# Kernel tuning notes

Measured on AMD Instinct MI355X. Metric: run time of the kernel, lower is better.

## Reference

```python
import jax, jax.numpy as jnp
import numpy as np

LN_EPS = 1e-5

def layer_norm(x, w, b):
    mu = jnp.mean(x, axis=-1, keepdims=True)
    var = jnp.var(x, axis=-1, keepdims=True)
    return (x - mu) * jax.lax.rsqrt(var + LN_EPS) * w + b

def masked_softmax_topk(ctx, k):
    # ctx: [B, D, D]; keep top-k per row (scatter-style mask), softmax over last dim
    B, D, _ = ctx.shape
    idx = jax.lax.top_k(ctx, k)[1]                       # [B, D, k]
    mask = jnp.zeros(ctx.shape, bool).at[
        jnp.arange(B)[:, None, None], jnp.arange(D)[None, :, None], idx
    ].set(True)
    return jax.nn.softmax(jnp.where(mask, ctx, -jnp.inf), axis=-1)

def setup_inputs() -> dict:
    key = jax.random.key(0)
    ks = jax.random.split(key, 8)
    B, H, W, C = 8, 96, 96, 256
    x1 = jax.random.normal(ks[0], (B, H, W, C), jnp.float32)
    x2 = jax.random.normal(ks[1], (B, H, W, C), jnp.float32)
    norm1_w = jnp.ones((C,), jnp.float32)
    norm1_b = jnp.zeros((C,), jnp.float32)
    reproj_w = jax.random.normal(ks[2], (2 * C, C), jnp.float32) * (1.0 / np.sqrt(C))  # 1x1 conv
    reproj_b = jnp.zeros((2 * C,), jnp.float32)
    norm2_w = jnp.ones((2 * C,), jnp.float32)
    norm2_b = jnp.zeros((2 * C,), jnp.float32)
    attn_w = jnp.full((4,), 0.25, jnp.float32)  # attn1..attn4 scalars
    return {"x1": x1, "x2": x2, "norm1_w": norm1_w, "norm1_b": norm1_b,
            "reproj_w": reproj_w, "reproj_b": reproj_b,
            "norm2_w": norm2_w, "norm2_b": norm2_b, "attn_w": attn_w}

def reference(x1, x2, norm1_w, norm1_b, reproj_w, reproj_b, norm2_w, norm2_b, attn_w):
    B, H, W, C = x1.shape
    N, D = H * W, C  # head_count = 1
    n1 = layer_norm(x1.reshape(B, N, C), norm1_w, norm1_b)   # values source
    n2 = layer_norm(x2.reshape(B, N, C), norm1_w, norm1_b)   # keys/queries source
    kq = jnp.swapaxes(n2, 1, 2)                              # [B, D, N]
    values = jnp.swapaxes(n1, 1, 2)                          # [B, D, N]
    keyv = jax.nn.softmax(kq, axis=2)                        # softmax over N
    query = jax.nn.softmax(kq, axis=1)                       # softmax over channels
    context = jnp.einsum('bdn,ben->bde', keyv, values)       # [B, D, D]
    ks = [D // 2, (D * 2) // 3, (D * 3) // 4, (D * 4) // 5]
    attended = jnp.zeros((B, D, N), x1.dtype)
    for i, k in enumerate(ks):
        attn = masked_softmax_topk(context, k)               # [B, D, D]
        attended = attended + attn_w[i] * jnp.einsum('bde,ben->bdn', attn, query)
    # 1x1 conv reprojection D -> 2D, then LayerNorm over 2D
    rp = jnp.einsum('od,bdn->bno', reproj_w, attended) + reproj_b  # [B, N, 2D]
    rp = layer_norm(rp, norm2_w, norm2_b)
    out = rp.reshape(B, H, W, 2 * C).transpose(0, 3, 1, 2)   # [B, 2C, H, W]
    return out
```

## Files before the change

### kernel.cpp

```cpp
#include <hip/hip_runtime.h>
#include <math.h>

typedef __attribute__((ext_vector_type(8))) short short8;
typedef __attribute__((ext_vector_type(4))) float f32x4;
typedef unsigned short u16;
typedef unsigned int u32;

constexpr int Bb = 8;
constexpr int Nn = 9216;
constexpr int Cc = 256;
constexpr int Oo = 512;
constexpr float LN_EPS = 1e-5f;
constexpr int KS2 = 8;

static __device__ __forceinline__ u16 f2bf(float f) {
    unsigned u = __builtin_bit_cast(unsigned, f);
    u += 0x7fffu + ((u >> 16) & 1u);
    return (u16)(u >> 16);
}
static __device__ __forceinline__ float bf2f(u16 u) {
    return __builtin_bit_cast(float, (unsigned)u << 16);
}

__global__ __launch_bounds__(512, 2) void k_pre(const float* __restrict__ src,
                                                const float* __restrict__ lnw,
                                                const float* __restrict__ lnb,
                                                u16* __restrict__ dstT,
                                                u16* __restrict__ Qexp,
                                                float* __restrict__ pS,
                                                int doExp) {
    __shared__ u16 tile[256][66];
    __shared__ float wsh[256], bsh[256];
    const int b = blockIdx.z;
    const int nc = (blockIdx.x & 7) * 18 + (blockIdx.x >> 3);
    const int n0 = nc * 64;
    const int t = threadIdx.x;
    if (t < 256) { wsh[t] = lnw[t]; bsh[t] = lnb[t]; }
    __syncthreads();

    const int r = t >> 3;
    const int g = t & 7;
    const long long row = (long long)b * Nn + n0 + r;
    const float* rowp = src + row * Cc;

    float4 v[8];
#pragma unroll
    for (int i = 0; i < 8; ++i)
        v[i] = *reinterpret_cast<const float4*>(rowp + g * 4 + i * 32);

    float s = 0.f, q = 0.f;
#pragma unroll
    for (int i = 0; i < 8; ++i) {
        s += v[i].x + v[i].y + v[i].z + v[i].w;
        q += v[i].x * v[i].x + v[i].y * v[i].y + v[i].z * v[i].z + v[i].w * v[i].w;
    }
    s += __shfl_xor(s, 1); s += __shfl_xor(s, 2); s += __shfl_xor(s, 4);
    q += __shfl_xor(q, 1); q += __shfl_xor(q, 2); q += __shfl_xor(q, 4);
    const float mu = s * (1.0f / Cc);
    const float rstd = rsqrtf(q * (1.0f / Cc) - mu * mu + LN_EPS);

    float se = 0.f;
#pragma unroll
    for (int i = 0; i < 8; ++i) {
        const int d = g * 4 + i * 32;
        const float4 w4 = *reinterpret_cast<const float4*>(&wsh[d]);
        const float4 b4 = *reinterpret_cast<const float4*>(&bsh[d]);
        v[i].x = (v[i].x - mu) * rstd * w4.x + b4.x;
        v[i].y = (v[i].y - mu) * rstd * w4.y + b4.y;
        v[i].z = (v[i].z - mu) * rstd * w4.z + b4.z;
        v[i].w = (v[i].w - mu) * rstd * w4.w + b4.w;
        if (doExp) {
            v[i].x = __expf(v[i].x); v[i].y = __expf(v[i].y);
            v[i].z = __expf(v[i].z); v[i].w = __expf(v[i].w);
            se += v[i].x + v[i].y + v[i].z + v[i].w;
        }
        tile[d + 0][r] = f2bf(v[i].x);
        tile[d + 1][r] = f2bf(v[i].y);
        tile[d + 2][r] = f2bf(v[i].z);
        tile[d + 3][r] = f2bf(v[i].w);
    }

    if (doExp) {
        se += __shfl_xor(se, 1); se += __shfl_xor(se, 2); se += __shfl_xor(se, 4);
        const float inv = 1.0f / se;
#pragma unroll
        for (int i = 0; i < 8; ++i) {
            const int d = g * 4 + i * 32;
            int2 pk;
            pk.x = (int)((unsigned)f2bf(v[i].x * inv) | ((unsigned)f2bf(v[i].y * inv) << 16));
            pk.y = (int)((unsigned)f2bf(v[i].z * inv) | ((unsigned)f2bf(v[i].w * inv) << 16));
            *reinterpret_cast<int2*>(Qexp + row * Cc + d) = pk;
        }
    }
    __syncthreads();

#pragma unroll
    for (int p = 0; p < 4; ++p) {
        const int d = p * 64 + (t >> 3);
        const int c = (t & 7) * 8;
        int4 u;
        u.x = (int)*reinterpret_cast<const u32*>(&tile[d][c + 0]);
        u.y = (int)*reinterpret_cast<const u32*>(&tile[d][c + 2]);
        u.z = (int)*reinterpret_cast<const u32*>(&tile[d][c + 4]);
        u.w = (int)*reinterpret_cast<const u32*>(&tile[d][c + 6]);
        *reinterpret_cast<int4*>(dstT + ((long long)(b * Cc + d)) * Nn + n0 + c) = u;
        if (doExp) {
            const unsigned uu[4] = {(unsigned)u.x, (unsigned)u.y, (unsigned)u.z, (unsigned)u.w};
            float ss = 0.f;
#pragma unroll
            for (int j = 0; j < 4; ++j) {
                ss += bf2f((u16)(uu[j] & 0xffff));
                ss += bf2f((u16)(uu[j] >> 16));
            }
            ss += __shfl_xor(ss, 1);
            ss += __shfl_xor(ss, 2);
            ss += __shfl_xor(ss, 4);
            if ((t & 7) == 0) pS[((long long)b * 144 + nc) * Cc + d] = ss;
        }
    }
}

__global__ __launch_bounds__(256) void k_colcomb(const float* __restrict__ pS,
                                                 float* __restrict__ colS) {
    const int d = threadIdx.x, b = blockIdx.x;
    float s = 0.f;
    for (int c = 0; c < 144; ++c) s += pS[((long long)b * 144 + c) * Cc + d];
    colS[b * Cc + d] = s;
}

__global__ __launch_bounds__(256) void k_mm_bf16(const u16* __restrict__ A,
                                                 const u16* __restrict__ Bt,
                                                 float* __restrict__ C,
                                                 int lda, int ldb, int ldc,
                                                 long long sAb, long long sBb, long long sCb,
                                                 int kChunk, long long sCk,
                                                 int tilesN, int kIters) {
    __shared__ alignas(16) unsigned char smemRaw[32768];
    u16* Asm = reinterpret_cast<u16*>(smemRaw);
    u16* Bsm = reinterpret_cast<u16*>(smemRaw + 16384);
    float (*patch)[16][68] = reinterpret_cast<float (*)[16][68]>(smemRaw);

    const int t = threadIdx.x;
    const int b = blockIdx.z, kc = blockIdx.y;
    const int tm = blockIdx.x / tilesN, tn = blockIdx.x % tilesN;
    const int m0 = tm * 128, n0 = tn * 128;
    const u16* Ag = A + b * sAb + (long long)kc * kChunk;
    const u16* Bg = Bt + b * sBb + (long long)kc * kChunk;
    float* Cg = C + b * sCb + (long long)kc * sCk;

    const int l = t & 63, w = t >> 6;
    const int wr = w >> 1, wc = w & 1;
    const int frow = l & 15, fk = (l >> 4) << 3;

    f32x4 acc[4][4] = {};

    for (int kt = 0; kt < kIters; ++kt) {
        const int k0 = kt * 64;
        int4 av[4], bv[4];
#pragma unroll
        for (int i = 0; i < 4; ++i) {
            const int s = t + 256 * i;
            const int r = s >> 3, c16 = s & 7;
            av[i] = *reinterpret_cast<const int4*>(Ag + (long long)(m0 + r) * lda + k0 + c16 * 8);
            bv[i] = *reinterpret_cast<const int4*>(Bg + (long long)(n0 + r) * ldb + k0 + c16 * 8);
        }
        __syncthreads();
#pragma unroll
        for (int i = 0; i < 4; ++i) {
            const int s = t + 256 * i;
            const int r = s >> 3, c16 = s & 7;
            const int idx = r * 64 + ((c16 * 8) ^ ((r & 7) << 3));
            *reinterpret_cast<int4*>(&Asm[idx]) = av[i];
            *reinterpret_cast<int4*>(&Bsm[idx]) = bv[i];
        }
        __syncthreads();
#pragma unroll
        for (int kf = 0; kf < 2; ++kf) {
            short8 af[4], bf[4];
            const int kk = kf * 32 + fk;
#pragma unroll
            for (int mi = 0; mi < 4; ++mi) {
                const int row = wr * 64 + mi * 16 + frow;
                af[mi] = *reinterpret_cast<const short8*>(&Asm[row * 64 + (kk ^ ((row & 7) << 3))]);
            }
#pragma unroll
            for (int ni = 0; ni < 4; ++ni) {
                const int row = wc * 64 + ni * 16 + frow;
                bf[ni] = *reinterpret_cast<const short8*>(&Bsm[row * 64 + (kk ^ ((row & 7) << 3))]);
            }
#pragma unroll
            for (int mi = 0; mi < 4; ++mi)
#pragma unroll
                for (int ni = 0; ni < 4; ++ni)
                    acc[mi][ni] = __builtin_amdgcn_mfma_f32_16x16x32_bf16(af[mi], bf[ni], acc[mi][ni], 0, 0, 0);
        }
    }

    __syncthreads();
    const int crow0 = (l >> 4) * 4, ccol = l & 15;
#pragma unroll
    for (int mi = 0; mi < 4; ++mi) {
#pragma unroll
        for (int ni = 0; ni < 4; ++ni)
#pragma unroll
            for (int r_ = 0; r_ < 4; ++r_)
                patch[w][crow0 + r_][ni * 16 + ccol] = acc[mi][ni][r_];
        asm volatile("s_waitcnt lgkmcnt(0)" ::: "memory");
        __builtin_amdgcn_sched_barrier(0);
#pragma unroll
        for (int row = 0; row < 16; ++row)
            Cg[(long long)(m0 + wr * 64 + mi * 16 + row) * ldc + n0 + wc * 64 + l] = patch[w][row][l];
        asm volatile("s_waitcnt lgkmcnt(0)" ::: "memory");
        __builtin_amdgcn_sched_barrier(0);
    }
}

__global__ __launch_bounds__(256) void k_ctxred(const float* __restrict__ ctxp,
                                                const float* __restrict__ colS,
                                                float* __restrict__ ctx) {
    const long long i4 = ((long long)blockIdx.x * 256 + threadIdx.x) * 4;
    float4 s = make_float4(0.f, 0.f, 0.f, 0.f);
    for (int kc = 0; kc < KS2; ++kc) {
        const float4 v = *reinterpret_cast<const float4*>(ctxp + (long long)kc * (Bb * Cc * Cc) + i4);
        s.x += v.x; s.y += v.y; s.z += v.z; s.w += v.w;
    }
    const int b = (int)(i4 >> 16);
    const int d = ((int)(i4 >> 8)) & 255;
    const float inv = 1.0f / colS[b * Cc + d];
    s.x *= inv; s.y *= inv; s.z *= inv; s.w *= inv;
    *reinterpret_cast<float4*>(ctx + i4) = s;
}

__global__ __launch_bounds__(256) void k_rank(const float* __restrict__ ctx,
                                              const float* __restrict__ aw,
                                              float* __restrict__ Ac) {
    __shared__ float row[256];
    __shared__ float red[256];
    const int d = blockIdx.x, b = blockIdx.y, e = threadIdx.x;
    const float c = ctx[((long long)(b * Cc + d)) * Cc + e];
    row[e] = c;
    __syncthreads();
    int p = 0;
    for (int j = 0; j < 256; ++j) {
        const float cj = row[j];
        p += (cj > c) || (cj == c && j < e);
    }
    red[e] = c; __syncthreads();
    for (int s_ = 128; s_; s_ >>= 1) { if (e < s_) red[e] = fmaxf(red[e], red[e + s_]); __syncthreads(); }
    const float m = red[0];
    const float ex = __expf(c - m);
    const int kks[4] = {128, 170, 192, 204};
    float Zv[4];
#pragma unroll
    for (int i = 0; i < 4; ++i) {
        __syncthreads();
        red[e] = (p < kks[i]) ? ex : 0.0f;
        __syncthreads();
        for (int s_ = 128; s_; s_ >>= 1) { if (e < s_) red[e] += red[e + s_]; __syncthreads(); }
        Zv[i] = red[0];
    }
    float wsum = 0.0f;
#pragma unroll
    for (int i = 0; i < 4; ++i)
        if (p < kks[i]) wsum += aw[i] / Zv[i];
    Ac[((long long)(b * Cc + d)) * Cc + e] = ex * wsum;
}

__global__ __launch_bounds__(256) void k_wa(const float* __restrict__ W,
                                            const float* __restrict__ Ac,
                                            u16* __restrict__ WAb16) {
    __shared__ float As[16][64], Bs[16][64];
    const int b = blockIdx.y;
    const int o0 = (blockIdx.x >> 2) * 64, e0 = (blockIdx.x & 3) * 64;
    const int t = threadIdx.x, tx = t & 15, ty = t >> 4;
    const int a_oo = t >> 2, a_k4 = (t & 3) * 4;
    const int b_kk = t >> 4, b_e4 = (t & 15) * 4;
    float acc[4][4] = {{0.f}};
    for (int kd = 0; kd < 256; kd += 16) {
        const float4 wv = *reinterpret_cast<const float4*>(W + (o0 + a_oo) * Cc + kd + a_k4);
        const float4 av = *reinterpret_cast<const float4*>(Ac + ((long long)(b * Cc + kd + b_kk)) * Cc + e0 + b_e4);
        __syncthreads();
        As[a_k4 + 0][a_oo] = wv.x; As[a_k4 + 1][a_oo] = wv.y;
        As[a_k4 + 2][a_oo] = wv.z; As[a_k4 + 3][a_oo] = wv.w;
        *reinterpret_cast<float4*>(&Bs[b_kk][b_e4]) = av;
        __syncthreads();
#pragma unroll
        for (int kk = 0; kk < 16; ++kk) {
            const float4 a4 = *reinterpret_cast<const float4*>(&As[kk][ty * 4]);
            const float4 b4 = *reinterpret_cast<const float4*>(&Bs[kk][tx * 4]);
            const float aa[4] = {a4.x, a4.y, a4.z, a4.w};
            const float bb[4] = {b4.x, b4.y, b4.z, b4.w};
#pragma unroll
            for (int i = 0; i < 4; ++i)
#pragma unroll
                for (int j = 0; j < 4; ++j) acc[i][j] = fmaf(aa[i], bb[j], acc[i][j]);
        }
    }
#pragma unroll
    for (int i = 0; i < 4; ++i) {
        int2 pk;
        pk.x = (int)((unsigned)f2bf(acc[i][0]) | ((unsigned)f2bf(acc[i][1]) << 16));
        pk.y = (int)((unsigned)f2bf(acc[i][2]) | ((unsigned)f2bf(acc[i][3]) << 16));
        *reinterpret_cast<int2*>(WAb16 + ((long long)(b * Oo + o0 + ty * 4 + i)) * Cc + e0 + tx * 4) = pk;
    }
}

__global__ __launch_bounds__(256, 3) void k_rpln(const u16* __restrict__ Qexp,
                                                 const u16* __restrict__ WAb16,
                                                 const float* __restrict__ rbias,
                                                 const float* __restrict__ nw,
                                                 const float* __restrict__ nb,
                                                 float* __restrict__ out) {
    __shared__ float patch[4][16][36];
    __shared__ float psum[32][4], psq[32][4];
    __shared__ float muA[32], rsA[32];

    const int t = threadIdx.x;
    const int b = blockIdx.z;
    const int nt_ = (blockIdx.x & 7) * 36 + (blockIdx.x >> 3);
    const int n0 = nt_ * 32;
    const int l = t & 63, w = t >> 6;
    const int frow = l & 15, fk = (l >> 4) << 3;
    const int hi = l >> 4;

    f32x4 acc[2][8] = {};

    const u16* Aq = Qexp + ((long long)b * Nn + n0) * Cc;
    const u16* Bw = WAb16 + ((long long)b * Oo + w * 128) * Cc;

    int4 aF[2][8];
#pragma unroll
    for (int mi = 0; mi < 2; ++mi)
#pragma unroll
        for (int s = 0; s < 8; ++s)
            aF[mi][s] = *reinterpret_cast<const int4*>(Aq + (mi * 16 + frow) * Cc + s * 32 + fk);

    int4 bC[8], bN[8];
#pragma unroll
    for (int ni = 0; ni < 8; ++ni)
        bC[ni] = *reinterpret_cast<const int4*>(Bw + (ni * 16 + frow) * Cc + fk);

#pragma unroll
    for (int s = 0; s < 8; ++s) {
        if (s < 7) {
            const int kk = (s + 1) * 32 + fk;
#pragma unroll
            for (int ni = 0; ni < 8; ++ni)
                bN[ni] = *reinterpret_cast<const int4*>(Bw + (ni * 16 + frow) * Cc + kk);
        }
#pragma unroll
        for (int mi = 0; mi < 2; ++mi)
#pragma unroll
            for (int ni = 0; ni < 8; ++ni)
                acc[mi][ni] = __builtin_amdgcn_mfma_f32_16x16x32_bf16(
                    __builtin_bit_cast(short8, aF[mi][s]), __builtin_bit_cast(short8, bC[ni]),
                    acc[mi][ni], 0, 0, 0);
        if (s < 7) {
#pragma unroll
            for (int ni = 0; ni < 8; ++ni) bC[ni] = bN[ni];
        }
    }

#pragma unroll
    for (int ni = 0; ni < 8; ++ni) {
        const float bb = rbias[w * 128 + ni * 16 + frow];
#pragma unroll
        for (int mi = 0; mi < 2; ++mi)
#pragma unroll
            for (int r_ = 0; r_ < 4; ++r_) acc[mi][ni][r_] += bb;
    }
#pragma unroll
    for (int mi = 0; mi < 2; ++mi)
#pragma unroll
        for (int r_ = 0; r_ < 4; ++r_) {
            float s = 0.f, q = 0.f;
#pragma unroll
            for (int ni = 0; ni < 8; ++ni) { const float v = acc[mi][ni][r_]; s += v; q += v * v; }
#pragma unroll
            for (int m = 8; m; m >>= 1) { s += __shfl_xor(s, m); q += __shfl_xor(q, m); }
            if (frow == 0) {
                const int row = mi * 16 + hi * 4 + r_;
                psum[row][w] = s; psq[row][w] = q;
            }
        }
    __syncthreads();
    if (t < 32) {
        const float s = psum[t][0] + psum[t][1] + psum[t][2] + psum[t][3];
        const float q = psq[t][0] + psq[t][1] + psq[t][2] + psq[t][3];
        const float m = s * (1.0f / Oo);
        muA[t] = m;
        rsA[t] = rsqrtf(q * (1.0f / Oo) - m * m + LN_EPS);
    }
    __syncthreads();

    float nwv[8], nbv[8];
#pragma unroll
    for (int ni = 0; ni < 8; ++ni) {
        const int o = w * 128 + ni * 16 + frow;
        nwv[ni] = nw[o]; nbv[ni] = nb[o];
    }

#pragma unroll
    for (int ni = 0; ni < 8; ++ni) {
#pragma unroll
        for (int mi = 0; mi < 2; ++mi)
#pragma unroll
            for (int r_ = 0; r_ < 4; ++r_) {
                const int nl = mi * 16 + hi * 4 + r_;
                patch[w][frow][nl] = (acc[mi][ni][r_] - muA[nl]) * rsA[nl] * nwv[ni] + nbv[ni];
            }
        asm volatile("s_waitcnt lgkmcnt(0)" ::: "memory");
        __builtin_amdgcn_sched_barrier(0);
#pragma unroll
        for (int p = 0; p < 2; ++p) {
            const int o_loc = p * 8 + (l >> 3);
            const int colf4 = l & 7;
            const f32x4 v = *reinterpret_cast<const f32x4*>(&patch[w][o_loc][colf4 * 4]);
            const int o_g = w * 128 + ni * 16 + o_loc;
            __builtin_nontemporal_store(v,
                reinterpret_cast<f32x4*>(&out[((long long)(b * Oo + o_g)) * Nn + n0 + colf4 * 4]));
        }
        asm volatile("s_waitcnt lgkmcnt(0)" ::: "memory");
        __builtin_amdgcn_sched_barrier(0);
    }
}

extern "C" void kernel_launch(void* const* d_in, const int* in_sizes, int n_in,
                              void* d_out, int out_size, void* d_ws, size_t ws_size,
                              hipStream_t stream) {
    (void)in_sizes; (void)n_in; (void)out_size; (void)ws_size;
    const float* x1    = (const float*)d_in[0];
    const float* x2    = (const float*)d_in[1];
    const float* n1w   = (const float*)d_in[2];
    const float* n1b   = (const float*)d_in[3];
    const float* rw    = (const float*)d_in[4];
    const float* rbias = (const float*)d_in[5];
    const float* n2w   = (const float*)d_in[6];
    const float* n2b   = (const float*)d_in[7];
    const float* aw    = (const float*)d_in[8];
    float* out = (float*)d_out;

    u16* KexpT = (u16*)d_out;
    u16* VT    = KexpT + (size_t)Bb * Nn * Cc;

    float* ws = (float*)d_ws;
    size_t off = 0;
    u16*   Qexp   = (u16*)(ws + off); off += (size_t)Bb * Nn * Cc / 2;
    float* ctxp   = ws + off; off += (size_t)KS2 * Bb * Cc * Cc;
    float* ctx    = ws + off; off += (size_t)Bb * Cc * Cc;
    float* Ac     = ws + off; off += (size_t)Bb * Cc * Cc;
    u16*   WAb16  = (u16*)(ws + off); off += (size_t)Bb * Oo * Cc / 2;
    float* pS     = ws + off; off += (size_t)Bb * 144 * Cc;
    float* colS   = ws + off; off += (size_t)Bb * Cc;

    k_pre<<<dim3(144, 1, Bb), 512, 0, stream>>>(x2, n1w, n1b, KexpT, Qexp, pS, 1);
    k_pre<<<dim3(144, 1, Bb), 512, 0, stream>>>(x1, n1w, n1b, VT, Qexp, pS, 0);
    k_colcomb<<<dim3(Bb), 256, 0, stream>>>(pS, colS);
    k_mm_bf16<<<dim3(4, KS2, Bb), 256, 0, stream>>>(
        KexpT, VT, ctxp,
        Nn, Nn, Cc,
        (long long)Cc * Nn, (long long)Cc * Nn, (long long)Cc * Cc,
        Nn / KS2, (long long)Bb * Cc * Cc,
        Cc / 128, (Nn / KS2) / 64);
    k_ctxred<<<dim3(512), 256, 0, stream>>>(ctxp, colS, ctx);
    k_rank<<<dim3(Cc, Bb), 256, 0, stream>>>(ctx, aw, Ac);
    k_wa<<<dim3(32, Bb), 256, 0, stream>>>(rw, Ac, WAb16);
    k_rpln<<<dim3(288, 1, Bb), 256, 0, stream>>>(Qexp, WAb16, rbias, n2w, n2b, out);
}
```

Baseline: 258.7 us.

## Store K/V row-major, drop Qexp buffer, fold row normalisation into reprojection

The preprocessing kernel now writes exp'd keys and values in row-major [N,C] bf16 instead of transposing through shared memory, and it no longer writes a separate row-normalised Qexp buffer. It stores per-row exp sums instead, and the reprojection kernel multiplies its output by the inverse row sum before adding the bias. The context GEMM transposes tiles while staging into shared memory, using scalar 16-bit LDS stores. This removes one full bf16 activation write and the LDS transpose in the prepass, at the cost of a more expensive shared-memory store pattern in the GEMM.

```diff
diff --git a/kernel.cpp b/kernel.cpp
--- a/kernel.cpp
+++ b/kernel.cpp
@@ -25,12 +25,12 @@
 __global__ __launch_bounds__(512, 2) void k_pre(const float* __restrict__ src,
                                                 const float* __restrict__ lnw,
                                                 const float* __restrict__ lnb,
-                                                u16* __restrict__ dstT,
-                                                u16* __restrict__ Qexp,
+                                                u16* __restrict__ dst,
+                                                float* __restrict__ rowsum,
                                                 float* __restrict__ pS,
                                                 int doExp) {
-    __shared__ u16 tile[256][66];
     __shared__ float wsh[256], bsh[256];
+    __shared__ float wred[8][256];
     const int b = blockIdx.z;
     const int nc = (blockIdx.x & 7) * 18 + (blockIdx.x >> 3);
     const int n0 = nc * 64;
@@ -40,6 +40,7 @@
 
     const int r = t >> 3;
     const int g = t & 7;
+    const int wv = t >> 6;
     const long long row = (long long)b * Nn + n0 + r;
     const float* rowp = src + row * Cc;
 
@@ -60,6 +61,7 @@
     const float rstd = rsqrtf(q * (1.0f / Cc) - mu * mu + LN_EPS);
 
     float se = 0.f;
+    u16 h[8][4];
 #pragma unroll
     for (int i = 0; i < 8; ++i) {
         const int d = g * 4 + i * 32;
@@ -74,48 +76,38 @@
             v[i].z = __expf(v[i].z); v[i].w = __expf(v[i].w);
             se += v[i].x + v[i].y + v[i].z + v[i].w;
         }
-        tile[d + 0][r] = f2bf(v[i].x);
-        tile[d + 1][r] = f2bf(v[i].y);
-        tile[d + 2][r] = f2bf(v[i].z);
-        tile[d + 3][r] = f2bf(v[i].w);
+        h[i][0] = f2bf(v[i].x); h[i][1] = f2bf(v[i].y);
+        h[i][2] = f2bf(v[i].z); h[i][3] = f2bf(v[i].w);
+        int2 pk;
+        pk.x = (int)((unsigned)h[i][0] | ((unsigned)h[i][1] << 16));
+        pk.y = (int)((unsigned)h[i][2] | ((unsigned)h[i][3] << 16));
+        *reinterpret_cast<int2*>(dst + row * Cc + d) = pk;
     }
 
     if (doExp) {
         se += __shfl_xor(se, 1); se += __shfl_xor(se, 2); se += __shfl_xor(se, 4);
-        const float inv = 1.0f / se;
+        if (g == 0) rowsum[row] = se;
 #pragma unroll
         for (int i = 0; i < 8; ++i) {
-            const int d = g * 4 + i * 32;
-            int2 pk;
-            pk.x = (int)((unsigned)f2bf(v[i].x * inv) | ((unsigned)f2bf(v[i].y * inv) << 16));
-            pk.y = (int)((unsigned)f2bf(v[i].z * inv) | ((unsigned)f2bf(v[i].w * inv) << 16));
-            *reinterpret_cast<int2*>(Qexp + row * Cc + d) = pk;
-        }
-    }
-    __syncthreads();
-
-#pragma unroll
-    for (int p = 0; p < 4; ++p) {
-        const int d = p * 64 + (t >> 3);
-        const int c = (t & 7) * 8;
-        int4 u;
-        u.x = (int)*reinterpret_cast<const u32*>(&tile[d][c + 0]);
-        u.y = (int)*reinterpret_cast<const u32*>(&tile[d][c + 2]);
-        u.z = (int)*reinterpret_cast<const u32*>(&tile[d][c + 4]);
-        u.w = (int)*reinterpret_cast<const u32*>(&tile[d][c + 6]);
-        *reinterpret_cast<int4*>(dstT + ((long long)(b * Cc + d)) * Nn + n0 + c) = u;
-        if (doExp) {
-            const unsigned uu[4] = {(unsigned)u.x, (unsigned)u.y, (unsigned)u.z, (unsigned)u.w};
+            float c0 = bf2f(h[i][0]), c1 = bf2f(h[i][1]);
+            float c2 = bf2f(h[i][2]), c3 = bf2f(h[i][3]);
+#pragma unroll
+            for (int m = 8; m <= 32; m <<= 1) {
+                c0 += __shfl_xor(c0, m); c1 += __shfl_xor(c1, m);
+                c2 += __shfl_xor(c2, m); c3 += __shfl_xor(c3, m);
+            }
+            if ((t & 63) < 8) {
+                const int d = g * 4 + i * 32;
+                wred[wv][d + 0] = c0; wred[wv][d + 1] = c1;
+                wred[wv][d + 2] = c2; wred[wv][d + 3] = c3;
+            }
+        }
+        __syncthreads();
+        if (t < 256) {
             float ss = 0.f;
 #pragma unroll
-            for (int j = 0; j < 4; ++j) {
-                ss += bf2f((u16)(uu[j] & 0xffff));
-                ss += bf2f((u16)(uu[j] >> 16));
-            }
-            ss += __shfl_xor(ss, 1);
-            ss += __shfl_xor(ss, 2);
-            ss += __shfl_xor(ss, 4);
-            if ((t & 7) == 0) pS[((long long)b * 144 + nc) * Cc + d] = ss;
+            for (int i = 0; i < 8; ++i) ss += wred[i][t];
+            pS[((long long)b * 144 + nc) * Cc + t] = ss;
         }
     }
 }
@@ -128,13 +120,9 @@
     colS[b * Cc + d] = s;
 }
 
-__global__ __launch_bounds__(256) void k_mm_bf16(const u16* __restrict__ A,
-                                                 const u16* __restrict__ Bt,
-                                                 float* __restrict__ C,
-                                                 int lda, int ldb, int ldc,
-                                                 long long sAb, long long sBb, long long sCb,
-                                                 int kChunk, long long sCk,
-                                                 int tilesN, int kIters) {
+__global__ __launch_bounds__(256) void k_ctx2(const u16* __restrict__ Kexp,
+                                              const u16* __restrict__ V,
+                                              float* __restrict__ ctxp) {
     __shared__ alignas(16) unsigned char smemRaw[32768];
     u16* Asm = reinterpret_cast<u16*>(smemRaw);
     u16* Bsm = reinterpret_cast<u16*>(smemRaw + 16384);
@@ -142,36 +130,35 @@
 
     const int t = threadIdx.x;
     const int b = blockIdx.z, kc = blockIdx.y;
-    const int tm = blockIdx.x / tilesN, tn = blockIdx.x % tilesN;
-    const int m0 = tm * 128, n0 = tn * 128;
-    const u16* Ag = A + b * sAb + (long long)kc * kChunk;
-    const u16* Bg = Bt + b * sBb + (long long)kc * kChunk;
-    float* Cg = C + b * sCb + (long long)kc * sCk;
-
+    const int d0 = (blockIdx.x >> 1) * 128, e0 = (blockIdx.x & 1) * 128;
     const int l = t & 63, w = t >> 6;
     const int wr = w >> 1, wc = w & 1;
     const int frow = l & 15, fk = (l >> 4) << 3;
+    const int sr = t & 63, sw = t >> 6;
 
     f32x4 acc[4][4] = {};
 
-    for (int kt = 0; kt < kIters; ++kt) {
-        const int k0 = kt * 64;
+    for (int kt = 0; kt < 18; ++kt) {
+        const long long nb = (long long)b * Nn + kc * 1152 + kt * 64;
         int4 av[4], bv[4];
 #pragma unroll
-        for (int i = 0; i < 4; ++i) {
-            const int s = t + 256 * i;
-            const int r = s >> 3, c16 = s & 7;
-            av[i] = *reinterpret_cast<const int4*>(Ag + (long long)(m0 + r) * lda + k0 + c16 * 8);
-            bv[i] = *reinterpret_cast<const int4*>(Bg + (long long)(n0 + r) * ldb + k0 + c16 * 8);
-        }
-        __syncthreads();
-#pragma unroll
-        for (int i = 0; i < 4; ++i) {
-            const int s = t + 256 * i;
-            const int r = s >> 3, c16 = s & 7;
-            const int idx = r * 64 + ((c16 * 8) ^ ((r & 7) << 3));
-            *reinterpret_cast<int4*>(&Asm[idx]) = av[i];
-            *reinterpret_cast<int4*>(&Bsm[idx]) = bv[i];
+        for (int j = 0; j < 4; ++j) {
+            const int c8 = sw * 4 + j;
+            av[j] = *reinterpret_cast<const int4*>(Kexp + (nb + sr) * Cc + d0 + c8 * 8);
+            bv[j] = *reinterpret_cast<const int4*>(V + (nb + sr) * Cc + e0 + c8 * 8);
+        }
+        __syncthreads();
+#pragma unroll
+        for (int j = 0; j < 4; ++j) {
+            const u16* pa = reinterpret_cast<const u16*>(&av[j]);
+            const u16* pb = reinterpret_cast<const u16*>(&bv[j]);
+#pragma unroll
+            for (int e8 = 0; e8 < 8; ++e8) {
+                const int dd = (sw * 4 + j) * 8 + e8;
+                const int col = sr ^ (e8 << 3);
+                Asm[dd * 64 + col] = pa[e8];
+                Bsm[dd * 64 + col] = pb[e8];
+            }
         }
         __syncthreads();
 #pragma unroll
@@ -180,13 +167,13 @@
             const int kk = kf * 32 + fk;
 #pragma unroll
             for (int mi = 0; mi < 4; ++mi) {
-                const int row = wr * 64 + mi * 16 + frow;
-                af[mi] = *reinterpret_cast<const short8*>(&Asm[row * 64 + (kk ^ ((row & 7) << 3))]);
+                const int rw_ = wr * 64 + mi * 16 + frow;
+                af[mi] = *reinterpret_cast<const short8*>(&Asm[rw_ * 64 + (kk ^ ((rw_ & 7) << 3))]);
             }
 #pragma unroll
             for (int ni = 0; ni < 4; ++ni) {
-                const int row = wc * 64 + ni * 16 + frow;
-                bf[ni] = *reinterpret_cast<const short8*>(&Bsm[row * 64 + (kk ^ ((row & 7) << 3))]);
+                const int rw_ = wc * 64 + ni * 16 + frow;
+                bf[ni] = *reinterpret_cast<const short8*>(&Bsm[rw_ * 64 + (kk ^ ((rw_ & 7) << 3))]);
             }
 #pragma unroll
             for (int mi = 0; mi < 4; ++mi)
@@ -197,6 +184,7 @@
     }
 
     __syncthreads();
+    float* Cg = ctxp + ((long long)kc * Bb + b) * Cc * Cc;
     const int crow0 = (l >> 4) * 4, ccol = l & 15;
 #pragma unroll
     for (int mi = 0; mi < 4; ++mi) {
@@ -209,7 +197,7 @@
         __builtin_amdgcn_sched_barrier(0);
 #pragma unroll
         for (int row = 0; row < 16; ++row)
-            Cg[(long long)(m0 + wr * 64 + mi * 16 + row) * ldc + n0 + wc * 64 + l] = patch[w][row][l];
+            Cg[(long long)(d0 + wr * 64 + mi * 16 + row) * Cc + e0 + wc * 64 + l] = patch[w][row][l];
         asm volatile("s_waitcnt lgkmcnt(0)" ::: "memory");
         __builtin_amdgcn_sched_barrier(0);
     }
@@ -305,7 +293,8 @@
     }
 }
 
-__global__ __launch_bounds__(256, 3) void k_rpln(const u16* __restrict__ Qexp,
+__global__ __launch_bounds__(256, 3) void k_rpln(const u16* __restrict__ Kexp,
+                                                 const float* __restrict__ rowsum,
                                                  const u16* __restrict__ WAb16,
                                                  const float* __restrict__ rbias,
                                                  const float* __restrict__ nw,
@@ -314,6 +303,7 @@
     __shared__ float patch[4][16][36];
     __shared__ float psum[32][4], psq[32][4];
     __shared__ float muA[32], rsA[32];
+    __shared__ float irow[32];
 
     const int t = threadIdx.x;
     const int b = blockIdx.z;
@@ -323,9 +313,11 @@
     const int frow = l & 15, fk = (l >> 4) << 3;
     const int hi = l >> 4;
 
+    if (t < 32) irow[t] = 1.0f / rowsum[(long long)b * Nn + n0 + t];
+
     f32x4 acc[2][8] = {};
 
-    const u16* Aq = Qexp + ((long long)b * Nn + n0) * Cc;
+    const u16* Aq = Kexp + ((long long)b * Nn + n0) * Cc;
     const u16* Bw = WAb16 + ((long long)b * Oo + w * 128) * Cc;
 
     int4 aF[2][8];
@@ -361,13 +353,17 @@
         }
     }
 
+    __syncthreads();
 #pragma unroll
     for (int ni = 0; ni < 8; ++ni) {
         const float bb = rbias[w * 128 + ni * 16 + frow];
 #pragma unroll
         for (int mi = 0; mi < 2; ++mi)
 #pragma unroll
-            for (int r_ = 0; r_ < 4; ++r_) acc[mi][ni][r_] += bb;
+            for (int r_ = 0; r_ < 4; ++r_) {
+                const int rw_ = mi * 16 + hi * 4 + r_;
+                acc[mi][ni][r_] = acc[mi][ni][r_] * irow[rw_] + bb;
+            }
     }
 #pragma unroll
     for (int mi = 0; mi < 2; ++mi)
@@ -440,30 +436,25 @@
     const float* aw    = (const float*)d_in[8];
     float* out = (float*)d_out;
 
-    u16* KexpT = (u16*)d_out;
-    u16* VT    = KexpT + (size_t)Bb * Nn * Cc;
+    u16* V = (u16*)d_out;
 
     float* ws = (float*)d_ws;
     size_t off = 0;
-    u16*   Qexp   = (u16*)(ws + off); off += (size_t)Bb * Nn * Cc / 2;
+    u16*   Kexp   = (u16*)(ws + off); off += (size_t)Bb * Nn * Cc / 2;
     float* ctxp   = ws + off; off += (size_t)KS2 * Bb * Cc * Cc;
     float* ctx    = ws + off; off += (size_t)Bb * Cc * Cc;
     float* Ac     = ws + off; off += (size_t)Bb * Cc * Cc;
     u16*   WAb16  = (u16*)(ws + off); off += (size_t)Bb * Oo * Cc / 2;
     float* pS     = ws + off; off += (size_t)Bb * 144 * Cc;
     float* colS   = ws + off; off += (size_t)Bb * Cc;
-
-    k_pre<<<dim3(144, 1, Bb), 512, 0, stream>>>(x2, n1w, n1b, KexpT, Qexp, pS, 1);
-    k_pre<<<dim3(144, 1, Bb), 512, 0, stream>>>(x1, n1w, n1b, VT, Qexp, pS, 0);
+    float* rowsum = ws + off; off += (size_t)Bb * Nn;
+
+    k_pre<<<dim3(144, 1, Bb), 512, 0, stream>>>(x2, n1w, n1b, Kexp, rowsum, pS, 1);
+    k_pre<<<dim3(144, 1, Bb), 512, 0, stream>>>(x1, n1w, n1b, V, rowsum, pS, 0);
     k_colcomb<<<dim3(Bb), 256, 0, stream>>>(pS, colS);
-    k_mm_bf16<<<dim3(4, KS2, Bb), 256, 0, stream>>>(
-        KexpT, VT, ctxp,
-        Nn, Nn, Cc,
-        (long long)Cc * Nn, (long long)Cc * Nn, (long long)Cc * Cc,
-        Nn / KS2, (long long)Bb * Cc * Cc,
-        Cc / 128, (Nn / KS2) / 64);
+    k_ctx2<<<dim3(4, KS2, Bb), 256, 0, stream>>>(Kexp, V, ctxp);
     k_ctxred<<<dim3(512), 256, 0, stream>>>(ctxp, colS, ctx);
     k_rank<<<dim3(Cc, Bb), 256, 0, stream>>>(ctx, aw, Ac);
     k_wa<<<dim3(32, Bb), 256, 0, stream>>>(rw, Ac, WAb16);
-    k_rpln<<<dim3(288, 1, Bb), 256, 0, stream>>>(Qexp, WAb16, rbias, n2w, n2b, out);
-}
+    k_rpln<<<dim3(288, 1, Bb), 256, 0, stream>>>(Kexp, rowsum, WAb16, rbias, n2w, n2b, out);
+}
```

New measurement: 229.7 us. 1.13x faster.
